# Kernel tuning notes

Hardware: AMD Instinct MI355X
Metric: run time of the kernel (lower is better)

Reference implementation:

```python
import jax, jax.numpy as jnp
import numpy as np
from jax import lax

B = 16384
NWIRES = 4


def _conv(x, w, b):
    # NCHW conv, stride 1, SAME padding (pad 1 for k=3)
    y = lax.conv_general_dilated(x, w, (1, 1), ((1, 1), (1, 1)),
                                 dimension_numbers=("NCHW", "OIHW", "NCHW"))
    return y + b[None, :, None, None]


def _pool2(x):
    b, c, h, w = x.shape
    return x.reshape(b, c, h // 2, 2, w // 2, 2).max(axis=(3, 5))


def _apply_1q(state, U, wire):
    # state: (B,2,2,2,2) complex; U: (B,2,2) complex
    s = jnp.moveaxis(state, wire + 1, -1)
    s = jnp.einsum("bij,b...j->b...i", U, s)
    return jnp.moveaxis(s, -1, wire + 1)


def _apply_cnot(state, c, t):
    s0 = jnp.take(state, 0, axis=c + 1)
    s1 = jnp.take(state, 1, axis=c + 1)
    ta = t + 1 if t < c else t  # target axis index after removing control axis
    s1 = jnp.flip(s1, axis=ta)
    return jnp.stack([s0, s1], axis=c + 1)


def _ry(th):
    c = jnp.cos(th / 2)
    s = jnp.sin(th / 2)
    U = jnp.stack([jnp.stack([c, -s], -1), jnp.stack([s, c], -1)], -2)
    return U.astype(jnp.complex64)


def _rz(th):
    e = jnp.exp(-0.5j * th.astype(jnp.complex64))
    z = jnp.zeros_like(e)
    return jnp.stack([jnp.stack([e, z], -1), jnp.stack([z, jnp.conj(e)], -1)], -2)


def _rx(th):
    c = jnp.cos(th / 2).astype(jnp.complex64)
    s = jnp.sin(th / 2).astype(jnp.complex64)
    return jnp.stack([jnp.stack([c, -1j * s], -1), jnp.stack([-1j * s, c], -1)], -2)


def _circuit(params):
    # params: (B, 16) -> PauliZ expvals (B, 4)
    b = params.shape[0]
    state = jnp.zeros((b, 16), jnp.complex64).at[:, 0].set(1.0).reshape(b, 2, 2, 2, 2)
    for i in range(NWIRES):
        state = _apply_1q(state, _ry(params[:, 4 * i + 0]), i)
        state = _apply_1q(state, _rz(params[:, 4 * i + 1]), i)
        state = _apply_1q(state, _rx(params[:, 4 * i + 2]), i)
        state = _apply_cnot(state, i, (i + 1) % NWIRES)
    probs = state.real ** 2 + state.imag ** 2  # (B,2,2,2,2)
    zs = []
    for i in range(NWIRES):
        p = probs.sum(axis=tuple(a for a in range(1, 5) if a != i + 1))  # (B,2)
        zs.append(p[:, 0] - p[:, 1])
    return jnp.stack(zs, axis=-1)


def setup_inputs() -> dict:
    key = jax.random.key(0)
    ks = jax.random.split(key, 12)
    d = {}
    d["x"] = jax.random.normal(ks[0], (B, 1, 28, 28), jnp.float32)
    d["conv1_w"] = jax.random.normal(ks[1], (4, 1, 3, 3), jnp.float32) * 0.3
    d["conv1_b"] = jax.random.normal(ks[2], (4,), jnp.float32) * 0.1
    d["conv2_w"] = jax.random.normal(ks[3], (4, 4, 3, 3), jnp.float32) * 0.15
    d["conv2_b"] = jax.random.normal(ks[4], (4,), jnp.float32) * 0.1
    d["pl_w"] = jax.random.normal(ks[5], (16, 196), jnp.float32) * 0.07
    d["pl_b"] = jax.random.normal(ks[6], (16,), jnp.float32) * 0.05
    d["ro_w"] = jax.random.normal(ks[7], (4, 4), jnp.float32) * 0.5
    d["ro_b"] = jax.random.normal(ks[8], (4,), jnp.float32) * 0.1
    d["bn_w"] = jnp.ones((4,), jnp.float32)
    d["bn_b"] = jnp.zeros((4,), jnp.float32)
    return d


def reference(x, conv1_w, conv1_b, conv2_w, conv2_b, pl_w, pl_b, ro_w, ro_b, bn_w, bn_b):
    h = _pool2(jax.nn.relu(_conv(x, conv1_w, conv1_b)))   # (B,4,14,14)
    h = _pool2(jax.nn.relu(_conv(h, conv2_w, conv2_b)))   # (B,4,7,7)
    flat = h.reshape(x.shape[0], -1)                      # (B,196)
    params = flat @ pl_w.T + pl_b                         # (B,16)
    z = _circuit(params)                                  # (B,4)
    out = z @ ro_w.T + ro_b                               # (B,4)
    mean = out.mean(0)
    var = out.var(0)  # biased, matches torch BN training normalization
    return (out - mean) / jnp.sqrt(var + 1e-5) * bn_w + bn_b
```

## Files before the change

kernel.cpp:

```cpp
#include <hip/hip_runtime.h>
#include <math.h>

#define BATCH 16384

typedef float v2f __attribute__((ext_vector_type(2)));

__device__ __forceinline__ v2f pk_fma(v2f a, v2f b, v2f c) {
  return __builtin_elementwise_fma(a, b, c);
}
__device__ __forceinline__ v2f pk_max(v2f a, v2f b) {
  return __builtin_elementwise_max(a, b);
}

__global__ __launch_bounds__(256) void qnat_fused(
    const float* __restrict__ x,
    const float* __restrict__ w1,
    const float* __restrict__ b1,
    const float* __restrict__ w2,
    const float* __restrict__ b2,
    const float* __restrict__ plw,
    const float* __restrict__ plb,
    const float* __restrict__ rw,
    const float* __restrict__ rb,
    float* __restrict__ pre,
    float* __restrict__ stats)
{
  __shared__ __align__(16) float h1p[4][4 * 288 + 16];
  __shared__ __align__(16) float h2[4][4][196];
  __shared__ float s_red[4][8];

  const int tid = threadIdx.x;
  const int w = tid >> 6;
  const int lane = tid & 63;
  const int wid = blockIdx.x * 4 + w;
  const int base = wid * 4;

  {
    float4 z4 = make_float4(0.f, 0.f, 0.f, 0.f);
    float4* hz = (float4*)&h1p[w][0];
    #pragma unroll
    for (int t = 0; t < 5; t++) {
      int p = t * 64 + lane;
      if (p < 292) hz[p] = z4;
    }
  }

  const int i = lane >> 2;
  const int q = lane & 3;
  const bool c1act = lane < 56;

  float4 pfa[4], pfb[4];
  #pragma unroll
  for (int r = 0; r < 4; r++) { pfa[r] = make_float4(0,0,0,0); pfb[r] = make_float4(0,0,0,0); }

  if (c1act) {
    const float* xb = x + (size_t)base * 784;
    #pragma unroll
    for (int r = 0; r < 4; r++) {
      int row = 2 * i - 1 + r;
      if (0 <= row && row < 28) {
        const float* rp = xb + row * 28;
        pfa[r] = *(const float4*)(rp + 8 * q);
        if (q < 3) pfb[r] = *(const float4*)(rp + 8 * q + 4);
      }
    }
  }

  for (int it = 0; it < 4; ++it) {
    const int sample = base + it;

    if (c1act) {
      const float* xb = x + (size_t)sample * 784;
      float win[4][10];
      #pragma unroll
      for (int r = 0; r < 4; r++) {
        int row = 2 * i - 1 + r;
        bool v = (0 <= row && row < 28);
        const float* rp = xb + row * 28;
        win[r][0] = (v && q > 0) ? rp[8 * q - 1] : 0.0f;
        win[r][1] = pfa[r].x; win[r][2] = pfa[r].y;
        win[r][3] = pfa[r].z; win[r][4] = pfa[r].w;
        win[r][5] = pfb[r].x; win[r][6] = pfb[r].y;
        win[r][7] = pfb[r].z; win[r][8] = pfb[r].w;
        win[r][9] = (v && q < 3) ? rp[8 * q + 8] : 0.0f;
      }
      if (it != 3) {
        const float* xn = x + (size_t)(sample + 1) * 784;
        #pragma unroll
        for (int r = 0; r < 4; r++) {
          int row = 2 * i - 1 + r;
          pfa[r] = make_float4(0,0,0,0);
          pfb[r] = make_float4(0,0,0,0);
          if (0 <= row && row < 28) {
            const float* rp = xn + row * 28;
            pfa[r] = *(const float4*)(rp + 8 * q);
            if (q < 3) pfb[r] = *(const float4*)(rp + 8 * q + 4);
          }
        }
      }
      v2f P[4][9];
      #pragma unroll
      for (int r = 0; r < 4; r++)
        #pragma unroll
        for (int k = 0; k < 9; k++) P[r][k] = (v2f){win[r][k], win[r][k + 1]};

      float* hb = &h1p[w][18 * (i + 1) + 1 + 4 * q];
      #pragma unroll
      for (int c = 0; c < 4; c++) {
        const float* wc = w1 + c * 9;
        const v2f bias2 = (v2f){b1[c], b1[c]};
        v2f a0[4], a1[4];
        #pragma unroll
        for (int jj = 0; jj < 4; jj++) { a0[jj] = bias2; a1[jj] = bias2; }
        #pragma unroll
        for (int dy = 0; dy < 3; dy++)
          #pragma unroll
          for (int dx = 0; dx < 3; dx++) {
            const float wv = wc[dy * 3 + dx];
            const v2f wvv = (v2f){wv, wv};
            #pragma unroll
            for (int jj = 0; jj < 4; jj++) {
              a0[jj] = pk_fma(P[dy][2 * jj + dx],     wvv, a0[jj]);
              a1[jj] = pk_fma(P[dy + 1][2 * jj + dx], wvv, a1[jj]);
            }
          }
        float m[4];
        #pragma unroll
        for (int jj = 0; jj < 4; jj++) {
          v2f mm = pk_max(a0[jj], a1[jj]);
          m[jj] = fmaxf(fmaxf(mm.x, mm.y), 0.0f);
        }
        float* p = hb + 288 * c;
        if (q < 3) {
          p[0] = m[0];
          *(float2*)(p + 1) = make_float2(m[1], m[2]);
          p[3] = m[3];
        } else {
          p[0] = m[0];
          p[1] = m[1];
        }
      }
    }

    {
      const int jq = lane & 7;
      const int i2 = lane >> 3;
      if (i2 < 7 && jq < 7) {
        v2f acc[4][2];
        #pragma unroll
        for (int co = 0; co < 4; co++) {
          const v2f bb = (v2f){b2[co], b2[co]};
          acc[co][0] = bb; acc[co][1] = bb;
        }
        #pragma unroll
        for (int ci = 0; ci < 4; ci++) {
          const float* rp = &h1p[w][288 * ci + 36 * i2 + 2 * jq];
          v2f Q[4][3];
          #pragma unroll
          for (int r = 0; r < 4; r++) {
            v2f a = *(const v2f*)(rp + 18 * r);
            v2f b = *(const v2f*)(rp + 18 * r + 2);
            Q[r][0] = a;
            Q[r][1] = (v2f){a.y, b.x};
            Q[r][2] = b;
          }
          #pragma unroll
          for (int co = 0; co < 4; co++) {
            const float* wp = w2 + (co * 4 + ci) * 9;
            #pragma unroll
            for (int dy = 0; dy < 3; dy++)
              #pragma unroll
              for (int dx = 0; dx < 3; dx++) {
                const float wv = wp[dy * 3 + dx];
                const v2f wvv = (v2f){wv, wv};
                acc[co][0] = pk_fma(Q[dy][dx],     wvv, acc[co][0]);
                acc[co][1] = pk_fma(Q[dy + 1][dx], wvv, acc[co][1]);
              }
          }
        }
        #pragma unroll
        for (int co = 0; co < 4; co++) {
          v2f mm = pk_max(acc[co][0], acc[co][1]);
          h2[w][it][49 * co + 7 * i2 + jq] = fmaxf(fmaxf(mm.x, mm.y), 0.0f);
        }
      }
    }
  }

  const int s2 = lane >> 4;
  const int k = lane & 15;

  float cv, sv;
  {
    const float4* hv4 = (const float4*)&h2[w][s2][0];
    const float4* wv4 = (const float4*)(plw + k * 196);
    v2f sacc = (v2f){0.0f, 0.0f};
    #pragma unroll 7
    for (int t = 0; t < 49; t++) {
      float4 hv = hv4[t];
      float4 wv = wv4[t];
      sacc = pk_fma((v2f){hv.x, hv.y}, (v2f){wv.x, wv.y}, sacc);
      sacc = pk_fma((v2f){hv.z, hv.w}, (v2f){wv.z, wv.w}, sacc);
    }
    float pv = sacc.x + sacc.y + plb[k];
    __sincosf(pv * 0.5f, &sv, &cv);
  }

  {
    const int l = k;
    const int gb = lane & 48;
    float re = (l == 0) ? 1.0f : 0.0f;
    float im = 0.0f;
    #pragma unroll
    for (int qi = 0; qi < 4; qi++) {
      const int beta = 3 - qi;
      const int m = 1 << beta;
      const int b = (l >> beta) & 1;
      float c = __shfl(cv, gb + 4 * qi, 64), s = __shfl(sv, gb + 4 * qi, 64);
      float pr_ = __shfl_xor(re, m, 64), pi_ = __shfl_xor(im, m, 64);
      float sg = b ? s : -s;
      re = fmaf(c, re, sg * pr_);
      im = fmaf(c, im, sg * pi_);
      c = __shfl(cv, gb + 4 * qi + 1, 64); s = __shfl(sv, gb + 4 * qi + 1, 64);
      float sz = b ? s : -s;
      float nr = c * re - sz * im;
      float ni = c * im + sz * re;
      re = nr; im = ni;
      c = __shfl(cv, gb + 4 * qi + 2, 64); s = __shfl(sv, gb + 4 * qi + 2, 64);
      pr_ = __shfl_xor(re, m, 64); pi_ = __shfl_xor(im, m, 64);
      nr = fmaf(c, re, s * pi_);
      ni = fmaf(c, im, -s * pr_);
      re = nr; im = ni;
      const int tm = 1 << (3 - ((qi + 1) & 3));
      float fr = __shfl_xor(re, tm, 64), fi = __shfl_xor(im, tm, 64);
      if (b) { re = fr; im = fi; }
    }
    float pr2 = re * re + im * im;
    float z0 = ((l >> 3) & 1) ? -pr2 : pr2;
    float z1 = ((l >> 2) & 1) ? -pr2 : pr2;
    float z2 = ((l >> 1) & 1) ? -pr2 : pr2;
    float z3 = (l & 1) ? -pr2 : pr2;
    #pragma unroll
    for (int off = 8; off >= 1; off >>= 1) {
      z0 += __shfl_xor(z0, off, 64);
      z1 += __shfl_xor(z1, off, 64);
      z2 += __shfl_xor(z2, off, 64);
      z3 += __shfl_xor(z3, off, 64);
    }
    float as0 = 0.f, as1 = 0.f, as2 = 0.f, as3 = 0.f;
    float aq0 = 0.f, aq1 = 0.f, aq2 = 0.f, aq3 = 0.f;
    if (l == 0) {
      float o0 = fmaf(rw[0],  z0, fmaf(rw[1],  z1, fmaf(rw[2],  z2, fmaf(rw[3],  z3, rb[0]))));
      float o1 = fmaf(rw[4],  z0, fmaf(rw[5],  z1, fmaf(rw[6],  z2, fmaf(rw[7],  z3, rb[1]))));
      float o2 = fmaf(rw[8],  z0, fmaf(rw[9],  z1, fmaf(rw[10], z2, fmaf(rw[11], z3, rb[2]))));
      float o3 = fmaf(rw[12], z0, fmaf(rw[13], z1, fmaf(rw[14], z2, fmaf(rw[15], z3, rb[3]))));
      *(float4*)(pre + (size_t)(base + s2) * 4) = make_float4(o0, o1, o2, o3);
      as0 = o0; aq0 = o0 * o0;
      as1 = o1; aq1 = o1 * o1;
      as2 = o2; aq2 = o2 * o2;
      as3 = o3; aq3 = o3 * o3;
    }
    #pragma unroll
    for (int off = 32; off >= 16; off >>= 1) {
      as0 += __shfl_down(as0, off, 64); aq0 += __shfl_down(aq0, off, 64);
      as1 += __shfl_down(as1, off, 64); aq1 += __shfl_down(aq1, off, 64);
      as2 += __shfl_down(as2, off, 64); aq2 += __shfl_down(aq2, off, 64);
      as3 += __shfl_down(as3, off, 64); aq3 += __shfl_down(aq3, off, 64);
    }
    if (lane == 0) {
      s_red[w][0] = as0; s_red[w][4] = aq0;
      s_red[w][1] = as1; s_red[w][5] = aq1;
      s_red[w][2] = as2; s_red[w][6] = aq2;
      s_red[w][3] = as3; s_red[w][7] = aq3;
    }
  }
  __syncthreads();
  if (tid < 8) {
    float v = s_red[0][tid] + s_red[1][tid] + s_red[2][tid] + s_red[3][tid];
    atomicAdd(&stats[tid], v);
  }
}

__global__ __launch_bounds__(256) void qnat_bn(
    float* __restrict__ pre,
    const float* __restrict__ stats,
    const float* __restrict__ bnw,
    const float* __restrict__ bnb)
{
  int idx = blockIdx.x * 256 + threadIdx.x;
  int c = idx & 3;
  float mean = stats[c] * (1.0f / BATCH);
  float ex2 = stats[4 + c] * (1.0f / BATCH);
  float var = ex2 - mean * mean;
  float inv = rsqrtf(var + 1e-5f);
  pre[idx] = (pre[idx] - mean) * inv * bnw[c] + bnb[c];
}

extern "C" void kernel_launch(void* const* d_in, const int* in_sizes, int n_in,
                              void* d_out, int out_size, void* d_ws, size_t ws_size,
                              hipStream_t stream) {
  const float* x   = (const float*)d_in[0];
  const float* w1  = (const float*)d_in[1];
  const float* b1  = (const float*)d_in[2];
  const float* w2  = (const float*)d_in[3];
  const float* b2  = (const float*)d_in[4];
  const float* plw = (const float*)d_in[5];
  const float* plb = (const float*)d_in[6];
  const float* rw  = (const float*)d_in[7];
  const float* rb  = (const float*)d_in[8];
  const float* bnw = (const float*)d_in[9];
  const float* bnb = (const float*)d_in[10];

  float* out   = (float*)d_out;
  float* stats = (float*)d_ws;

  hipMemsetAsync(stats, 0, 8 * sizeof(float), stream);
  qnat_fused<<<BATCH / 16, 256, 0, stream>>>(x, w1, b1, w2, b2, plw, plb, rw, rb, out, stats);
  qnat_bn<<<(BATCH * 4) / 256, 256, 0, stream>>>(out, stats, bnw, bnb);
}
```

Measured before the change: 138.2 us.

## Stage projection weights as bf16 in LDS and prefetch conv halo elements

Each block converts the 16x196 projection weights to packed bf16 once, stores them in shared memory in a transposed, padded layout, and reads them from there in the projection dot product instead of from global memory. The per-sample halo loads for conv1 are also moved into the prefetch stage, so they issue together with the next sample's float4 loads. The h2 row is padded to 200 floats and zero-filled so the unrolled loop can read whole 8-element chunks. This adds a block-wide barrier and per-block conversion work, and rounding the weights to bf16 loses precision in the circuit parameters.

```diff
diff --git a/kernel.cpp b/kernel.cpp
--- a/kernel.cpp
+++ b/kernel.cpp
@@ -10,6 +10,14 @@
 }
 __device__ __forceinline__ v2f pk_max(v2f a, v2f b) {
   return __builtin_elementwise_max(a, b);
+}
+
+__device__ __forceinline__ unsigned bf2(float lo, float hi) {
+  unsigned a = __float_as_uint(lo);
+  unsigned b = __float_as_uint(hi);
+  a = (a + 0x7fffu + ((a >> 16) & 1u)) >> 16;
+  b = (b + 0x7fffu + ((b >> 16) & 1u)) & 0xffff0000u;
+  return a | b;
 }
 
 __global__ __launch_bounds__(256) void qnat_fused(
@@ -26,14 +34,28 @@
     float* __restrict__ stats)
 {
   __shared__ __align__(16) float h1p[4][4 * 288 + 16];
-  __shared__ __align__(16) float h2[4][4][196];
+  __shared__ __align__(16) float h2[4][4][200];
+  __shared__ __align__(16) uint4 plw_tb[25 * 16];
   __shared__ float s_red[4][8];
 
   const int tid = threadIdx.x;
   const int w = tid >> 6;
   const int lane = tid & 63;
-  const int wid = blockIdx.x * 4 + w;
-  const int base = wid * 4;
+  const int base = (blockIdx.x * 4 + w) * 4;
+
+  #pragma unroll
+  for (int j = 0; j < 2; j++) {
+    int s = tid + 256 * j;
+    if (s < 400) {
+      int tp = s >> 4;
+      int k = s & 15;
+      const float4* pr = (const float4*)(plw + k * 196);
+      float4 a = pr[2 * tp];
+      float4 b = (tp < 24) ? pr[2 * tp + 1] : make_float4(0.f, 0.f, 0.f, 0.f);
+      plw_tb[s] = make_uint4(bf2(a.x, a.y), bf2(a.z, a.w),
+                             bf2(b.x, b.y), bf2(b.z, b.w));
+    }
+  }
 
   {
     float4 z4 = make_float4(0.f, 0.f, 0.f, 0.f);
@@ -43,15 +65,21 @@
       int p = t * 64 + lane;
       if (p < 292) hz[p] = z4;
     }
-  }
+    if (lane < 16) h2[w][lane >> 2][196 + (lane & 3)] = 0.0f;
+  }
+  __syncthreads();
 
   const int i = lane >> 2;
   const int q = lane & 3;
   const bool c1act = lane < 56;
 
   float4 pfa[4], pfb[4];
+  float pe0[4], pe1[4];
   #pragma unroll
-  for (int r = 0; r < 4; r++) { pfa[r] = make_float4(0,0,0,0); pfb[r] = make_float4(0,0,0,0); }
+  for (int r = 0; r < 4; r++) {
+    pfa[r] = make_float4(0,0,0,0); pfb[r] = make_float4(0,0,0,0);
+    pe0[r] = 0.0f; pe1[r] = 0.0f;
+  }
 
   if (c1act) {
     const float* xb = x + (size_t)base * 784;
@@ -61,40 +89,43 @@
       if (0 <= row && row < 28) {
         const float* rp = xb + row * 28;
         pfa[r] = *(const float4*)(rp + 8 * q);
-        if (q < 3) pfb[r] = *(const float4*)(rp + 8 * q + 4);
+        if (q > 0) pe0[r] = rp[8 * q - 1];
+        if (q < 3) {
+          pfb[r] = *(const float4*)(rp + 8 * q + 4);
+          pe1[r] = rp[8 * q + 8];
+        }
       }
     }
   }
 
   for (int it = 0; it < 4; ++it) {
-    const int sample = base + it;
-
     if (c1act) {
-      const float* xb = x + (size_t)sample * 784;
       float win[4][10];
       #pragma unroll
       for (int r = 0; r < 4; r++) {
-        int row = 2 * i - 1 + r;
-        bool v = (0 <= row && row < 28);
-        const float* rp = xb + row * 28;
-        win[r][0] = (v && q > 0) ? rp[8 * q - 1] : 0.0f;
+        win[r][0] = pe0[r];
         win[r][1] = pfa[r].x; win[r][2] = pfa[r].y;
         win[r][3] = pfa[r].z; win[r][4] = pfa[r].w;
         win[r][5] = pfb[r].x; win[r][6] = pfb[r].y;
         win[r][7] = pfb[r].z; win[r][8] = pfb[r].w;
-        win[r][9] = (v && q < 3) ? rp[8 * q + 8] : 0.0f;
+        win[r][9] = pe1[r];
       }
       if (it != 3) {
-        const float* xn = x + (size_t)(sample + 1) * 784;
+        const float* xn = x + (size_t)(base + it + 1) * 784;
         #pragma unroll
         for (int r = 0; r < 4; r++) {
           int row = 2 * i - 1 + r;
           pfa[r] = make_float4(0,0,0,0);
           pfb[r] = make_float4(0,0,0,0);
+          pe0[r] = 0.0f; pe1[r] = 0.0f;
           if (0 <= row && row < 28) {
             const float* rp = xn + row * 28;
             pfa[r] = *(const float4*)(rp + 8 * q);
-            if (q < 3) pfb[r] = *(const float4*)(rp + 8 * q + 4);
+            if (q > 0) pe0[r] = rp[8 * q - 1];
+            if (q < 3) {
+              pfb[r] = *(const float4*)(rp + 8 * q + 4);
+              pe1[r] = rp[8 * q + 8];
+            }
           }
         }
       }
@@ -193,14 +224,21 @@
   float cv, sv;
   {
     const float4* hv4 = (const float4*)&h2[w][s2][0];
-    const float4* wv4 = (const float4*)(plw + k * 196);
+    const uint4*  wb4 = &plw_tb[k];
     v2f sacc = (v2f){0.0f, 0.0f};
-    #pragma unroll 7
-    for (int t = 0; t < 49; t++) {
-      float4 hv = hv4[t];
-      float4 wv = wv4[t];
-      sacc = pk_fma((v2f){hv.x, hv.y}, (v2f){wv.x, wv.y}, sacc);
-      sacc = pk_fma((v2f){hv.z, hv.w}, (v2f){wv.z, wv.w}, sacc);
+    #pragma unroll
+    for (int t = 0; t < 25; t++) {
+      float4 h0 = hv4[2 * t];
+      float4 h1 = hv4[2 * t + 1];
+      uint4 wb = wb4[16 * t];
+      v2f w01 = (v2f){__uint_as_float(wb.x << 16), __uint_as_float(wb.x & 0xffff0000u)};
+      v2f w23 = (v2f){__uint_as_float(wb.y << 16), __uint_as_float(wb.y & 0xffff0000u)};
+      v2f w45 = (v2f){__uint_as_float(wb.z << 16), __uint_as_float(wb.z & 0xffff0000u)};
+      v2f w67 = (v2f){__uint_as_float(wb.w << 16), __uint_as_float(wb.w & 0xffff0000u)};
+      sacc = pk_fma((v2f){h0.x, h0.y}, w01, sacc);
+      sacc = pk_fma((v2f){h0.z, h0.w}, w23, sacc);
+      sacc = pk_fma((v2f){h1.x, h1.y}, w45, sacc);
+      sacc = pk_fma((v2f){h1.z, h1.w}, w67, sacc);
     }
     float pv = sacc.x + sacc.y + plb[k];
     __sincosf(pv * 0.5f, &sv, &cv);
```

Result: faster. 133.4 us, median of 2 (-3.5%).
